# Kernel tuning notes

Hardware: AMD Instinct MI355X
Metric: run time of the kernel (lower is better)

## Reference

```python
import jax, jax.numpy as jnp
import numpy as np

B, E, H, T = 16384, 1024, 16, 256  # batch, embed_dim, num_heads, tabular_dim
HD = E // H  # head_dim


def _mha_seq1(q, kv, Wqkv, bqkv, Wo, bo):
    """nn.MultiheadAttention with query/key/value of seq_len 1 (batch_first).
    q, kv: [B, E]; Wqkv: [3E, E]; bqkv: [3E]; Wo: [E, E]; bo: [E]."""
    Wq, Wk, Wv = jnp.split(Wqkv, 3, axis=0)
    bq, bk, bv = jnp.split(bqkv, 3)
    qp = (q @ Wq.T + bq).reshape(-1, H, HD)   # [B, H, HD]
    kp = (kv @ Wk.T + bk).reshape(-1, H, HD)
    vp = (kv @ Wv.T + bv).reshape(-1, H, HD)
    scores = jnp.sum(qp * kp, axis=-1, keepdims=True) * (1.0 / HD ** 0.5)  # [B, H, 1]
    w = jax.nn.softmax(scores, axis=-1)       # softmax over 1 key -> all ones
    out = (w * vp).reshape(-1, E)             # [B, E]
    return out @ Wo.T + bo


def setup_inputs() -> dict:
    key = jax.random.key(0)
    ks = jax.random.split(key, 16)
    s_e = 1.0 / E ** 0.5
    s_t = 1.0 / T ** 0.5
    return {
        "text_features": jax.random.normal(ks[0], (B, E), jnp.float32),
        "ecg_features": jax.random.normal(ks[1], (B, E), jnp.float32),
        "tabular_features": jax.random.normal(ks[2], (B, T), jnp.float32),
        "Wc_text": jax.random.uniform(ks[3], (E, T), jnp.float32, -s_t, s_t),
        "bc_text": jax.random.uniform(ks[4], (E,), jnp.float32, -s_t, s_t),
        "Wc_ecg": jax.random.uniform(ks[5], (E, T), jnp.float32, -s_t, s_t),
        "bc_ecg": jax.random.uniform(ks[6], (E,), jnp.float32, -s_t, s_t),
        "Wqkv_a": jax.random.uniform(ks[7], (3 * E, E), jnp.float32, -s_e, s_e),
        "bqkv_a": jnp.zeros((3 * E,), jnp.float32),
        "Wo_a": jax.random.uniform(ks[8], (E, E), jnp.float32, -s_e, s_e),
        "bo_a": jnp.zeros((E,), jnp.float32),
        "Wqkv_b": jax.random.uniform(ks[9], (3 * E, E), jnp.float32, -s_e, s_e),
        "bqkv_b": jnp.zeros((3 * E,), jnp.float32),
        "Wo_b": jax.random.uniform(ks[10], (E, E), jnp.float32, -s_e, s_e),
        "bo_b": jnp.zeros((E,), jnp.float32),
    }


def reference(text_features, ecg_features, tabular_features,
              Wc_text, bc_text, Wc_ecg, bc_ecg,
              Wqkv_a, bqkv_a, Wo_a, bo_a,
              Wqkv_b, bqkv_b, Wo_b, bo_b):
    text_scale = jax.nn.sigmoid(tabular_features @ Wc_text.T + bc_text)
    ecg_scale = jax.nn.sigmoid(tabular_features @ Wc_ecg.T + bc_ecg)
    text_query = text_features * text_scale
    ecg_query = ecg_features * ecg_scale
    attn_a = _mha_seq1(text_query, ecg_features, Wqkv_a, bqkv_a, Wo_a, bo_a)
    attn_b = _mha_seq1(ecg_query, text_features, Wqkv_b, bqkv_b, Wo_b, bo_b)
    return jnp.concatenate([attn_a, attn_b], axis=-1)
```

## Files before the change

kernel.cpp:

```cpp
#include <hip/hip_runtime.h>
#include <hip/hip_bf16.h>
#include <stdint.h>

typedef __bf16 bf16_t;
typedef bf16_t bf16x8 __attribute__((ext_vector_type(8)));
typedef bf16_t bf16x4 __attribute__((ext_vector_type(4)));
typedef float  f32x4  __attribute__((ext_vector_type(4)));

#define E_DIM 1024
#define B_ROWS 16384

__device__ __forceinline__ void gload_lds16(const void* g, void* l) {
    __builtin_amdgcn_global_load_lds(
        (const __attribute__((address_space(1))) void*)g,
        (__attribute__((address_space(3))) void*)l,
        16, 0, 0);
}

__global__ __launch_bounds__(256) void cvt_w2_k(const float* __restrict__ Wo_a,
                                                const float* __restrict__ Wo_b,
                                                bf16_t* __restrict__ out) {
    const int n4 = (E_DIM * E_DIM) / 4;
    int i = blockIdx.x * blockDim.x + threadIdx.x;
    const float* src = (i < n4) ? Wo_a : Wo_b;
    int j = (i < n4) ? i : i - n4;
    f32x4 v = ((const f32x4*)src)[j];
    bf16x4 o;
    o[0] = (bf16_t)v[0]; o[1] = (bf16_t)v[1];
    o[2] = (bf16_t)v[2]; o[3] = (bf16_t)v[3];
    ((bf16x4*)out)[i] = o;
}

__global__ __launch_bounds__(256) void transpose_cvt2_k(const float* __restrict__ Wqkv_a,
                                                        const float* __restrict__ Wqkv_b,
                                                        bf16_t* __restrict__ out) {
    const size_t MAT = (size_t)E_DIM * E_DIM;
    int b = blockIdx.x;
    int ms = b >> 8;
    const float* in = (ms ? Wqkv_b : Wqkv_a) + 2 * MAT;
    bf16_t* o = out + (size_t)ms * MAT;
    int bb = b & 255;
    __shared__ float t[64][65];
    int bx = bb & 15;
    int by = bb >> 4;
    int j0 = by * 64, k0 = bx * 64;
    int tid = threadIdx.x;
#pragma unroll
    for (int p = 0; p < 4; ++p) {
        int u = tid + 256 * p;
        int r = u >> 4, c4 = u & 15;
        f32x4 v = *(const f32x4*)(in + (size_t)(j0 + r) * E_DIM + k0 + c4 * 4);
        t[r][c4 * 4 + 0] = v[0]; t[r][c4 * 4 + 1] = v[1];
        t[r][c4 * 4 + 2] = v[2]; t[r][c4 * 4 + 3] = v[3];
    }
    __syncthreads();
#pragma unroll
    for (int p = 0; p < 4; ++p) {
        int u = tid + 256 * p;
        int r = u >> 4, c4 = u & 15;
        bf16x4 ov;
        ov[0] = (bf16_t)t[c4 * 4 + 0][r];
        ov[1] = (bf16_t)t[c4 * 4 + 1][r];
        ov[2] = (bf16_t)t[c4 * 4 + 2][r];
        ov[3] = (bf16_t)t[c4 * 4 + 3][r];
        *(bf16x4*)(o + (size_t)(k0 + r) * E_DIM + j0 + c4 * 4) = ov;
    }
}

__global__ void fuse_bias2_k(const float* __restrict__ Wo_a, const float* __restrict__ bqkv_a,
                             const float* __restrict__ bo_a,
                             const float* __restrict__ Wo_b, const float* __restrict__ bqkv_b,
                             const float* __restrict__ bo_b, float* __restrict__ beff) {
    int idx = blockIdx.x;
    int sel = idx >> 10;
    int i = idx & 1023;
    const float* Wo = sel ? Wo_b : Wo_a;
    const float* bv = (sel ? bqkv_b : bqkv_a) + 2 * E_DIM;
    const float* bo = sel ? bo_b : bo_a;
    float s = 0.f;
    for (int j = threadIdx.x; j < E_DIM; j += 64)
        s += Wo[(size_t)i * E_DIM + j] * bv[j];
#pragma unroll
    for (int o = 32; o > 0; o >>= 1) s += __shfl_down(s, o);
    if (threadIdx.x == 0) beff[sel * E_DIM + i] = s + bo[i];
}

__global__ __launch_bounds__(256, 2) void fuse_gemm_k(const bf16_t* __restrict__ WoB,
                                                      const bf16_t* __restrict__ WvT,
                                                      bf16_t* __restrict__ Weff) {
    const size_t MAT = (size_t)E_DIM * E_DIM;
    int bid = blockIdx.x;
    int ms = bid >> 6;
    int t  = bid & 63;
    int mt = t >> 3, nt = t & 7;
    const bf16_t* A  = WoB + (size_t)ms * MAT;
    const bf16_t* Bm = WvT + (size_t)ms * MAT;
    bf16_t*       C  = Weff + (size_t)ms * MAT;
    int m0 = mt * 128, n0 = nt * 128;

    __shared__ __align__(16) bf16_t As[128][64];
    __shared__ __align__(16) bf16_t Bs[128][64];

    int tid = threadIdx.x;
    int lane = tid & 63;
    int wid = tid >> 6;
    int wrow = (wid >> 1) * 64;
    int wcol = (wid & 1) * 64;
    int cl = lane & 15;
    int rg = lane >> 4;

    f32x4 acc[4][4] = {};

    for (int kt = 0; kt < 16; ++kt) {
#pragma unroll
        for (int i = 0; i < 4; ++i) {
            int chunk = i * 256 + wid * 64 + lane;
            int row = chunk >> 3;
            int kk8 = (chunk & 7) * 8;
            char* la = (char*)(&As[0][0]) + (size_t)(i * 256 + wid * 64) * 16;
            char* lb = (char*)(&Bs[0][0]) + (size_t)(i * 256 + wid * 64) * 16;
            gload_lds16(A  + (size_t)(m0 + row) * E_DIM + kt * 64 + kk8, la);
            gload_lds16(Bm + (size_t)(n0 + row) * E_DIM + kt * 64 + kk8, lb);
        }
        __syncthreads();
#pragma unroll
        for (int ks = 0; ks < 2; ++ks) {
            int kk = ks * 32 + rg * 8;
            bf16x8 af[4], bq[4];
#pragma unroll
            for (int m = 0; m < 4; ++m) af[m] = *(const bf16x8*)(&As[wrow + m * 16 + cl][kk]);
#pragma unroll
            for (int n = 0; n < 4; ++n) bq[n] = *(const bf16x8*)(&Bs[wcol + n * 16 + cl][kk]);
#pragma unroll
            for (int m = 0; m < 4; ++m)
#pragma unroll
                for (int n = 0; n < 4; ++n)
                    acc[m][n] = __builtin_amdgcn_mfma_f32_16x16x32_bf16(af[m], bq[n], acc[m][n], 0, 0, 0);
        }
        __syncthreads();
    }

#pragma unroll
    for (int m = 0; m < 4; ++m) {
        int r = m0 + wrow + m * 16 + rg * 4;
#pragma unroll
        for (int n = 0; n < 4; ++n) {
            int c = n0 + wcol + n * 16 + cl;
#pragma unroll
            for (int j = 0; j < 4; ++j)
                C[(size_t)(r + j) * E_DIM + c] = (bf16_t)acc[m][n][j];
        }
    }
}

__global__ __launch_bounds__(256) void cvt_x2_k(const float* __restrict__ ecg,
                                                const float* __restrict__ text,
                                                bf16_t* __restrict__ out) {
    const int half = (B_ROWS * E_DIM) / 8;
    const int total = 2 * half;
    int stride = gridDim.x * blockDim.x;
    for (int i = blockIdx.x * blockDim.x + threadIdx.x; i < total; i += stride) {
        const float* src = (i < half) ? ecg : text;
        int j = (i < half) ? i : i - half;
        f32x4 lo = ((const f32x4*)src)[2 * j];
        f32x4 hi = ((const f32x4*)src)[2 * j + 1];
        bf16x8 v;
        v[0] = (bf16_t)lo[0]; v[1] = (bf16_t)lo[1]; v[2] = (bf16_t)lo[2]; v[3] = (bf16_t)lo[3];
        v[4] = (bf16_t)hi[0]; v[5] = (bf16_t)hi[1]; v[6] = (bf16_t)hi[2]; v[7] = (bf16_t)hi[3];
        ((bf16x8*)out)[i] = v;
    }
}

#define VMW(n) asm volatile("s_waitcnt vmcnt(" #n ")" ::: "memory")
#define BAR()  __builtin_amdgcn_s_barrier()

__global__ __launch_bounds__(512, 2) void main_gemm_256_k(const bf16_t* __restrict__ Xb,
                                                          const bf16_t* __restrict__ Weff,
                                                          const float* __restrict__ beff,
                                                          float* __restrict__ out) {
    const size_t MAT  = (size_t)E_DIM * E_DIM;
    const size_t XMAT = (size_t)B_ROWS * E_DIM;

    int bid = blockIdx.x;
    int wg = (bid & 7) * 64 + (bid >> 3);
    int nt = wg & 7;
    int mt = wg >> 3;
    int sel = nt >> 2;
    int n0 = (nt & 3) * 256;
    int m0 = mt * 256;

    const bf16_t* gA = Xb + (size_t)sel * XMAT + (size_t)m0 * E_DIM;
    const bf16_t* gB = Weff + (size_t)sel * MAT + (size_t)n0 * E_DIM;
    const float*  bb = beff + sel * E_DIM;

    __shared__ __align__(16) bf16_t sA[2][256 * 64];
    __shared__ __align__(16) bf16_t sB[2][256 * 64];

    int tid  = threadIdx.x;
    int lane = tid & 63;
    int wid  = tid >> 6;
    int wr = wid >> 2;
    int wc = wid & 3;
    int cl = lane & 15;
    int rg = lane >> 4;
    int wr16cl = wr * 16 + cl;
    int wc16cl = wc * 16 + cl;

    int c0 = tid, c1 = 512 + tid;
    int r0 = c0 >> 3, r1 = c1 >> 3;
    int go0 = r0 * E_DIM + (((c0 & 7) * 8) ^ ((r0 & 7) << 3));
    int go1 = r1 * E_DIM + (((c1 & 7) * 8) ^ ((r1 & 7) << 3));
    int ld0 = c0 * 8, ld1 = c1 * 8;

    int koff0 = (rg * 8) ^ ((cl & 7) << 3);
    int koff1 = (32 + rg * 8) ^ ((cl & 7) << 3);

    f32x4 acc[8][4] = {};
    bf16x8 af[4][2], bq[2][2];

#define STAGE_A(kt, h, prt) do { \
    gload_lds16(gA + (size_t)((h) * 128) * E_DIM + (kt) * 64 + go0, &sA[prt][(h) * 8192 + ld0]); \
    gload_lds16(gA + (size_t)((h) * 128) * E_DIM + (kt) * 64 + go1, &sA[prt][(h) * 8192 + ld1]); } while (0)
#define STAGE_B(kt, h, prt) do { \
    gload_lds16(gB + (size_t)((h) * 128) * E_DIM + (kt) * 64 + go0, &sB[prt][(h) * 8192 + ld0]); \
    gload_lds16(gB + (size_t)((h) * 128) * E_DIM + (kt) * 64 + go1, &sB[prt][(h) * 8192 + ld1]); } while (0)
#define RD_A(p, mh) do { _Pragma("unroll") for (int m = 0; m < 4; ++m) { \
    af[m][0] = *(const bf16x8*)(&sA[p][((mh) * 128 + m * 32 + wr16cl) * 64 + koff0]); \
    af[m][1] = *(const bf16x8*)(&sA[p][((mh) * 128 + m * 32 + wr16cl) * 64 + koff1]); } } while (0)
#define RD_B(p, nh) do { _Pragma("unroll") for (int n = 0; n < 2; ++n) { \
    bq[n][0] = *(const bf16x8*)(&sB[p][((nh) * 128 + n * 64 + wc16cl) * 64 + koff0]); \
    bq[n][1] = *(const bf16x8*)(&sB[p][((nh) * 128 + n * 64 + wc16cl) * 64 + koff1]); } } while (0)
#define MM(mh, nh) do { __builtin_amdgcn_s_setprio(1); \
    _Pragma("unroll") for (int m = 0; m < 4; ++m) _Pragma("unroll") for (int n = 0; n < 2; ++n) { \
        acc[(mh) * 4 + m][(nh) * 2 + n] = __builtin_amdgcn_mfma_f32_16x16x32_bf16(af[m][0], bq[n][0], acc[(mh) * 4 + m][(nh) * 2 + n], 0, 0, 0); \
        acc[(mh) * 4 + m][(nh) * 2 + n] = __builtin_amdgcn_mfma_f32_16x16x32_bf16(af[m][1], bq[n][1], acc[(mh) * 4 + m][(nh) * 2 + n], 0, 0, 0); } \
    __builtin_amdgcn_s_setprio(0); } while (0)

    STAGE_A(0, 0, 0); STAGE_B(0, 0, 0); STAGE_B(0, 1, 0); STAGE_A(0, 1, 0);
    VMW(4);
    BAR();

#pragma unroll
    for (int t = 0; t < 16; ++t) {
        const int p = t & 1, pn = p ^ 1;
        RD_A(p, 0); RD_B(p, 0);
        if (t < 15) { STAGE_A(t + 1, 0, pn); VMW(4); } else { VMW(2); }
        BAR();
        MM(0, 0);
        BAR();
        RD_B(p, 1);
        if (t < 15) { STAGE_B(t + 1, 0, pn); VMW(4); } else { VMW(0); }
        BAR();
        MM(0, 1);
        BAR();
        RD_A(p, 1);
        if (t < 15) STAGE_B(t + 1, 1, pn);
        BAR();
        MM(1, 1);
        BAR();
        RD_B(p, 0);
        if (t < 15) { STAGE_A(t + 1, 1, pn); VMW(4); }
        BAR();
        MM(1, 0);
        BAR();
    }

#pragma unroll
    for (int mi = 0; mi < 8; ++mi) {
        int r = m0 + mi * 32 + wr * 16 + rg * 4;
#pragma unroll
        for (int n = 0; n < 4; ++n) {
            int ch = n0 + n * 64 + wc16cl;
            float bias = bb[ch];
            size_t gc = (size_t)sel * E_DIM + ch;
#pragma unroll
            for (int j = 0; j < 4; ++j)
                out[(size_t)(r + j) * (2 * E_DIM) + gc] = acc[mi][n][j] + bias;
        }
    }
#undef STAGE_A
#undef STAGE_B
#undef RD_A
#undef RD_B
#undef MM
}

extern "C" void kernel_launch(void* const* d_in, const int* in_sizes, int n_in,
                              void* d_out, int out_size, void* d_ws, size_t ws_size,
                              hipStream_t stream) {
    const float* text   = (const float*)d_in[0];
    const float* ecg    = (const float*)d_in[1];
    const float* Wqkv_a = (const float*)d_in[7];
    const float* bqkv_a = (const float*)d_in[8];
    const float* Wo_a   = (const float*)d_in[9];
    const float* bo_a   = (const float*)d_in[10];
    const float* Wqkv_b = (const float*)d_in[11];
    const float* bqkv_b = (const float*)d_in[12];
    const float* Wo_b   = (const float*)d_in[13];
    const float* bo_b   = (const float*)d_in[14];

    const size_t MAT  = (size_t)E_DIM * E_DIM;
    const size_t XMAT = (size_t)B_ROWS * E_DIM;
    bf16_t* WoB  = (bf16_t*)d_ws;
    bf16_t* WvT  = WoB + 2 * MAT;
    bf16_t* Weff = WvT + 2 * MAT;
    float*  beff = (float*)(Weff + 2 * MAT);
    bf16_t* Xb   = (bf16_t*)(beff + 2 * E_DIM);

    cvt_x2_k<<<4096, 256, 0, stream>>>(ecg, text, Xb);
    cvt_w2_k<<<2048, 256, 0, stream>>>(Wo_a, Wo_b, WoB);
    transpose_cvt2_k<<<512, 256, 0, stream>>>(Wqkv_a, Wqkv_b, WvT);
    fuse_gemm_k<<<128, 256, 0, stream>>>(WoB, WvT, Weff);
    fuse_bias2_k<<<2048, 64, 0, stream>>>(Wo_a, bqkv_a, bo_a, Wo_b, bqkv_b, bo_b, beff);
    main_gemm_256_k<<<512, 512, 0, stream>>>(Xb, Weff, beff, (float*)d_out);
}
```

Baseline: 158.5 us.

## Fuse activation bf16 conversion into main GEMM and merge weight-prep kernels

The main GEMM now loads fp32 text/ecg rows straight into registers two k-tiles ahead, converts them to bf16 and writes them into swizzled LDS. This removes the separate activation-conversion kernel and its bf16 round-trip through global memory. The three small weight-prep kernels (Wo convert, Wv transpose, bias fold) are merged into one launch to cut launch overhead. In exchange, A traffic into the GEMM doubles in bytes, register pressure rises from the prefetch buffers, and the pipeline schedule is reworked.

```diff
diff --git a/kernel.cpp b/kernel.cpp
--- a/kernel.cpp
+++ b/kernel.cpp
@@ -17,72 +17,74 @@
         16, 0, 0);
 }
 
-__global__ __launch_bounds__(256) void cvt_w2_k(const float* __restrict__ Wo_a,
-                                                const float* __restrict__ Wo_b,
-                                                bf16_t* __restrict__ out) {
-    const int n4 = (E_DIM * E_DIM) / 4;
-    int i = blockIdx.x * blockDim.x + threadIdx.x;
-    const float* src = (i < n4) ? Wo_a : Wo_b;
-    int j = (i < n4) ? i : i - n4;
-    f32x4 v = ((const f32x4*)src)[j];
-    bf16x4 o;
-    o[0] = (bf16_t)v[0]; o[1] = (bf16_t)v[1];
-    o[2] = (bf16_t)v[2]; o[3] = (bf16_t)v[3];
-    ((bf16x4*)out)[i] = o;
-}
-
-__global__ __launch_bounds__(256) void transpose_cvt2_k(const float* __restrict__ Wqkv_a,
-                                                        const float* __restrict__ Wqkv_b,
-                                                        bf16_t* __restrict__ out) {
+__global__ __launch_bounds__(256) void prep_misc_k(const float* __restrict__ Wqkv_a,
+                                                   const float* __restrict__ bqkv_a,
+                                                   const float* __restrict__ Wo_a,
+                                                   const float* __restrict__ bo_a,
+                                                   const float* __restrict__ Wqkv_b,
+                                                   const float* __restrict__ bqkv_b,
+                                                   const float* __restrict__ Wo_b,
+                                                   const float* __restrict__ bo_b,
+                                                   bf16_t* __restrict__ WoB,
+                                                   bf16_t* __restrict__ WvT,
+                                                   float* __restrict__ beff) {
     const size_t MAT = (size_t)E_DIM * E_DIM;
+    __shared__ float t[64][65];
     int b = blockIdx.x;
-    int ms = b >> 8;
-    const float* in = (ms ? Wqkv_b : Wqkv_a) + 2 * MAT;
-    bf16_t* o = out + (size_t)ms * MAT;
-    int bb = b & 255;
-    __shared__ float t[64][65];
-    int bx = bb & 15;
-    int by = bb >> 4;
-    int j0 = by * 64, k0 = bx * 64;
     int tid = threadIdx.x;
-#pragma unroll
-    for (int p = 0; p < 4; ++p) {
-        int u = tid + 256 * p;
-        int r = u >> 4, c4 = u & 15;
-        f32x4 v = *(const f32x4*)(in + (size_t)(j0 + r) * E_DIM + k0 + c4 * 4);
-        t[r][c4 * 4 + 0] = v[0]; t[r][c4 * 4 + 1] = v[1];
-        t[r][c4 * 4 + 2] = v[2]; t[r][c4 * 4 + 3] = v[3];
-    }
-    __syncthreads();
-#pragma unroll
-    for (int p = 0; p < 4; ++p) {
-        int u = tid + 256 * p;
-        int r = u >> 4, c4 = u & 15;
-        bf16x4 ov;
-        ov[0] = (bf16_t)t[c4 * 4 + 0][r];
-        ov[1] = (bf16_t)t[c4 * 4 + 1][r];
-        ov[2] = (bf16_t)t[c4 * 4 + 2][r];
-        ov[3] = (bf16_t)t[c4 * 4 + 3][r];
-        *(bf16x4*)(o + (size_t)(k0 + r) * E_DIM + j0 + c4 * 4) = ov;
-    }
-}
-
-__global__ void fuse_bias2_k(const float* __restrict__ Wo_a, const float* __restrict__ bqkv_a,
-                             const float* __restrict__ bo_a,
-                             const float* __restrict__ Wo_b, const float* __restrict__ bqkv_b,
-                             const float* __restrict__ bo_b, float* __restrict__ beff) {
-    int idx = blockIdx.x;
-    int sel = idx >> 10;
-    int i = idx & 1023;
-    const float* Wo = sel ? Wo_b : Wo_a;
-    const float* bv = (sel ? bqkv_b : bqkv_a) + 2 * E_DIM;
-    const float* bo = sel ? bo_b : bo_a;
-    float s = 0.f;
-    for (int j = threadIdx.x; j < E_DIM; j += 64)
-        s += Wo[(size_t)i * E_DIM + j] * bv[j];
-#pragma unroll
-    for (int o = 32; o > 0; o >>= 1) s += __shfl_down(s, o);
-    if (threadIdx.x == 0) beff[sel * E_DIM + i] = s + bo[i];
+    if (b < 2048) {
+        const int n4 = (int)(MAT / 4);
+        int i = b * 256 + tid;
+        const float* src = (i < n4) ? Wo_a : Wo_b;
+        int j = (i < n4) ? i : i - n4;
+        f32x4 v = ((const f32x4*)src)[j];
+        bf16x4 o;
+        o[0] = (bf16_t)v[0]; o[1] = (bf16_t)v[1];
+        o[2] = (bf16_t)v[2]; o[3] = (bf16_t)v[3];
+        ((bf16x4*)WoB)[i] = o;
+    } else if (b < 2560) {
+        int x = b - 2048;
+        int ms = x >> 8;
+        const float* in = (ms ? Wqkv_b : Wqkv_a) + 2 * MAT;
+        bf16_t* o = WvT + (size_t)ms * MAT;
+        int bb = x & 255;
+        int bx = bb & 15, by = bb >> 4;
+        int j0 = by * 64, k0 = bx * 64;
+#pragma unroll
+        for (int p = 0; p < 4; ++p) {
+            int u = tid + 256 * p;
+            int r = u >> 4, c4 = u & 15;
+            f32x4 v = *(const f32x4*)(in + (size_t)(j0 + r) * E_DIM + k0 + c4 * 4);
+            t[r][c4 * 4 + 0] = v[0]; t[r][c4 * 4 + 1] = v[1];
+            t[r][c4 * 4 + 2] = v[2]; t[r][c4 * 4 + 3] = v[3];
+        }
+        __syncthreads();
+#pragma unroll
+        for (int p = 0; p < 4; ++p) {
+            int u = tid + 256 * p;
+            int r = u >> 4, c4 = u & 15;
+            bf16x4 ov;
+            ov[0] = (bf16_t)t[c4 * 4 + 0][r];
+            ov[1] = (bf16_t)t[c4 * 4 + 1][r];
+            ov[2] = (bf16_t)t[c4 * 4 + 2][r];
+            ov[3] = (bf16_t)t[c4 * 4 + 3][r];
+            *(bf16x4*)(o + (size_t)(k0 + r) * E_DIM + j0 + c4 * 4) = ov;
+        }
+    } else {
+        int idx = (b - 2560) * 4 + (tid >> 6);
+        int lane = tid & 63;
+        int sel = idx >> 10;
+        int i = idx & 1023;
+        const float* Wo = sel ? Wo_b : Wo_a;
+        const float* bv = (sel ? bqkv_b : bqkv_a) + 2 * E_DIM;
+        const float* bo = sel ? bo_b : bo_a;
+        float s = 0.f;
+        for (int j = lane; j < E_DIM; j += 64)
+            s += Wo[(size_t)i * E_DIM + j] * bv[j];
+#pragma unroll
+        for (int o = 32; o > 0; o >>= 1) s += __shfl_down(s, o);
+        if (lane == 0) beff[sel * E_DIM + i] = s + bo[i];
+    }
 }
 
 __global__ __launch_bounds__(256, 2) void fuse_gemm_k(const bf16_t* __restrict__ WoB,
@@ -153,33 +155,16 @@
     }
 }
 
-__global__ __launch_bounds__(256) void cvt_x2_k(const float* __restrict__ ecg,
-                                                const float* __restrict__ text,
-                                                bf16_t* __restrict__ out) {
-    const int half = (B_ROWS * E_DIM) / 8;
-    const int total = 2 * half;
-    int stride = gridDim.x * blockDim.x;
-    for (int i = blockIdx.x * blockDim.x + threadIdx.x; i < total; i += stride) {
-        const float* src = (i < half) ? ecg : text;
-        int j = (i < half) ? i : i - half;
-        f32x4 lo = ((const f32x4*)src)[2 * j];
-        f32x4 hi = ((const f32x4*)src)[2 * j + 1];
-        bf16x8 v;
-        v[0] = (bf16_t)lo[0]; v[1] = (bf16_t)lo[1]; v[2] = (bf16_t)lo[2]; v[3] = (bf16_t)lo[3];
-        v[4] = (bf16_t)hi[0]; v[5] = (bf16_t)hi[1]; v[6] = (bf16_t)hi[2]; v[7] = (bf16_t)hi[3];
-        ((bf16x8*)out)[i] = v;
-    }
-}
-
-#define VMW(n) asm volatile("s_waitcnt vmcnt(" #n ")" ::: "memory")
-#define BAR()  __builtin_amdgcn_s_barrier()
-
-__global__ __launch_bounds__(512, 2) void main_gemm_256_k(const bf16_t* __restrict__ Xb,
+#define VMW(n)  asm volatile("s_waitcnt vmcnt(" #n ")" ::: "memory")
+#define LGKM0() asm volatile("s_waitcnt lgkmcnt(0)" ::: "memory")
+#define BAR()   __builtin_amdgcn_s_barrier()
+
+__global__ __launch_bounds__(512, 2) void main_gemm_f32_k(const float* __restrict__ text,
+                                                          const float* __restrict__ ecg,
                                                           const bf16_t* __restrict__ Weff,
                                                           const float* __restrict__ beff,
                                                           float* __restrict__ out) {
-    const size_t MAT  = (size_t)E_DIM * E_DIM;
-    const size_t XMAT = (size_t)B_ROWS * E_DIM;
+    const size_t MAT = (size_t)E_DIM * E_DIM;
 
     int bid = blockIdx.x;
     int wg = (bid & 7) * 64 + (bid >> 3);
@@ -189,7 +174,7 @@
     int n0 = (nt & 3) * 256;
     int m0 = mt * 256;
 
-    const bf16_t* gA = Xb + (size_t)sel * XMAT + (size_t)m0 * E_DIM;
+    const float*  gA = (sel ? text : ecg) + (size_t)m0 * E_DIM;
     const bf16_t* gB = Weff + (size_t)sel * MAT + (size_t)n0 * E_DIM;
     const float*  bb = beff + sel * E_DIM;
 
@@ -208,61 +193,73 @@
 
     int c0 = tid, c1 = 512 + tid;
     int r0 = c0 >> 3, r1 = c1 >> 3;
-    int go0 = r0 * E_DIM + (((c0 & 7) * 8) ^ ((r0 & 7) << 3));
-    int go1 = r1 * E_DIM + (((c1 & 7) * 8) ^ ((r1 & 7) << 3));
+    int sc0 = ((c0 & 7) * 8) ^ ((r0 & 7) << 3);
+    int go0 = r0 * E_DIM + sc0;
+    int go1 = r1 * E_DIM + sc0;
     int ld0 = c0 * 8, ld1 = c1 * 8;
 
     int koff0 = (rg * 8) ^ ((cl & 7) << 3);
     int koff1 = (32 + rg * 8) ^ ((cl & 7) << 3);
 
     f32x4 acc[8][4] = {};
-    bf16x8 af[4][2], bq[2][2];
-
-#define STAGE_A(kt, h, prt) do { \
-    gload_lds16(gA + (size_t)((h) * 128) * E_DIM + (kt) * 64 + go0, &sA[prt][(h) * 8192 + ld0]); \
-    gload_lds16(gA + (size_t)((h) * 128) * E_DIM + (kt) * 64 + go1, &sA[prt][(h) * 8192 + ld1]); } while (0)
+    bf16x8 af[4][2], bqs[2][2], bq[2][2];
+    f32x4 pa[2][4];
+
 #define STAGE_B(kt, h, prt) do { \
     gload_lds16(gB + (size_t)((h) * 128) * E_DIM + (kt) * 64 + go0, &sB[prt][(h) * 8192 + ld0]); \
     gload_lds16(gB + (size_t)((h) * 128) * E_DIM + (kt) * 64 + go1, &sB[prt][(h) * 8192 + ld1]); } while (0)
+#define LOAD_A(kt, h) do { \
+    const float* _p0 = gA + (size_t)((h) * 128 + r0) * E_DIM + (kt) * 64 + sc0; \
+    const float* _p1 = gA + (size_t)((h) * 128 + 64 + r0) * E_DIM + (kt) * 64 + sc0; \
+    pa[h][0] = *(const f32x4*)_p0; pa[h][1] = *(const f32x4*)(_p0 + 4); \
+    pa[h][2] = *(const f32x4*)_p1; pa[h][3] = *(const f32x4*)(_p1 + 4); } while (0)
+#define CVT_A(h, prt) do { \
+    bf16x8 _v0, _v1; \
+    _v0[0] = (bf16_t)pa[h][0][0]; _v0[1] = (bf16_t)pa[h][0][1]; \
+    _v0[2] = (bf16_t)pa[h][0][2]; _v0[3] = (bf16_t)pa[h][0][3]; \
+    _v0[4] = (bf16_t)pa[h][1][0]; _v0[5] = (bf16_t)pa[h][1][1]; \
+    _v0[6] = (bf16_t)pa[h][1][2]; _v0[7] = (bf16_t)pa[h][1][3]; \
+    _v1[0] = (bf16_t)pa[h][2][0]; _v1[1] = (bf16_t)pa[h][2][1]; \
+    _v1[2] = (bf16_t)pa[h][2][2]; _v1[3] = (bf16_t)pa[h][2][3]; \
+    _v1[4] = (bf16_t)pa[h][3][0]; _v1[5] = (bf16_t)pa[h][3][1]; \
+    _v1[6] = (bf16_t)pa[h][3][2]; _v1[7] = (bf16_t)pa[h][3][3]; \
+    *(bf16x8*)(&sA[prt][(h) * 8192 + ld0]) = _v0; \
+    *(bf16x8*)(&sA[prt][(h) * 8192 + ld1]) = _v1; } while (0)
 #define RD_A(p, mh) do { _Pragma("unroll") for (int m = 0; m < 4; ++m) { \
     af[m][0] = *(const bf16x8*)(&sA[p][((mh) * 128 + m * 32 + wr16cl) * 64 + koff0]); \
     af[m][1] = *(const bf16x8*)(&sA[p][((mh) * 128 + m * 32 + wr16cl) * 64 + koff1]); } } while (0)
-#define RD_B(p, nh) do { _Pragma("unroll") for (int n = 0; n < 2; ++n) { \
-    bq[n][0] = *(const bf16x8*)(&sB[p][((nh) * 128 + n * 64 + wc16cl) * 64 + koff0]); \
-    bq[n][1] = *(const bf16x8*)(&sB[p][((nh) * 128 + n * 64 + wc16cl) * 64 + koff1]); } } while (0)
-#define MM(mh, nh) do { __builtin_amdgcn_s_setprio(1); \
+#define RD_B(p, nh, DST) do { _Pragma("unroll") for (int n = 0; n < 2; ++n) { \
+    DST[n][0] = *(const bf16x8*)(&sB[p][((nh) * 128 + n * 64 + wc16cl) * 64 + koff0]); \
+    DST[n][1] = *(const bf16x8*)(&sB[p][((nh) * 128 + n * 64 + wc16cl) * 64 + koff1]); } } while (0)
+#define MM(mh, nh, BQ) do { __builtin_amdgcn_s_setprio(1); \
     _Pragma("unroll") for (int m = 0; m < 4; ++m) _Pragma("unroll") for (int n = 0; n < 2; ++n) { \
-        acc[(mh) * 4 + m][(nh) * 2 + n] = __builtin_amdgcn_mfma_f32_16x16x32_bf16(af[m][0], bq[n][0], acc[(mh) * 4 + m][(nh) * 2 + n], 0, 0, 0); \
-        acc[(mh) * 4 + m][(nh) * 2 + n] = __builtin_amdgcn_mfma_f32_16x16x32_bf16(af[m][1], bq[n][1], acc[(mh) * 4 + m][(nh) * 2 + n], 0, 0, 0); } \
+        acc[(mh) * 4 + m][(nh) * 2 + n] = __builtin_amdgcn_mfma_f32_16x16x32_bf16(af[m][0], BQ[n][0], acc[(mh) * 4 + m][(nh) * 2 + n], 0, 0, 0); \
+        acc[(mh) * 4 + m][(nh) * 2 + n] = __builtin_amdgcn_mfma_f32_16x16x32_bf16(af[m][1], BQ[n][1], acc[(mh) * 4 + m][(nh) * 2 + n], 0, 0, 0); } \
     __builtin_amdgcn_s_setprio(0); } while (0)
 
-    STAGE_A(0, 0, 0); STAGE_B(0, 0, 0); STAGE_B(0, 1, 0); STAGE_A(0, 1, 0);
-    VMW(4);
+    LOAD_A(0, 0); LOAD_A(0, 1);
+    STAGE_B(0, 0, 0); STAGE_B(0, 1, 0);
+    CVT_A(0, 0); CVT_A(1, 0);
+    LOAD_A(1, 0); LOAD_A(1, 1);
+    VMW(8);
+    LGKM0();
     BAR();
 
 #pragma unroll
     for (int t = 0; t < 16; ++t) {
         const int p = t & 1, pn = p ^ 1;
-        RD_A(p, 0); RD_B(p, 0);
-        if (t < 15) { STAGE_A(t + 1, 0, pn); VMW(4); } else { VMW(2); }
-        BAR();
-        MM(0, 0);
-        BAR();
-        RD_B(p, 1);
-        if (t < 15) { STAGE_B(t + 1, 0, pn); VMW(4); } else { VMW(0); }
-        BAR();
-        MM(0, 1);
-        BAR();
+        RD_A(p, 0); RD_B(p, 0, bqs);
+        BAR(); MM(0, 0, bqs); BAR();
+        RD_B(p, 1, bq);
+        if (t < 15) { STAGE_B(t + 1, 0, pn); CVT_A(0, pn); }
+        BAR(); MM(0, 1, bq); BAR();
         RD_A(p, 1);
-        if (t < 15) STAGE_B(t + 1, 1, pn);
-        BAR();
-        MM(1, 1);
-        BAR();
-        RD_B(p, 0);
-        if (t < 15) { STAGE_A(t + 1, 1, pn); VMW(4); }
-        BAR();
-        MM(1, 0);
-        BAR();
+        if (t < 15) { STAGE_B(t + 1, 1, pn); CVT_A(1, pn); }
+        BAR(); MM(1, 1, bq); BAR();
+        if (t < 14) { LOAD_A(t + 2, 0); LOAD_A(t + 2, 1); VMW(8); }
+        else if (t == 14) { VMW(0); }
+        LGKM0();
+        BAR(); MM(1, 0, bqs); BAR();
     }
 
 #pragma unroll
@@ -278,8 +275,9 @@
                 out[(size_t)(r + j) * (2 * E_DIM) + gc] = acc[mi][n][j] + bias;
         }
     }
-#undef STAGE_A
 #undef STAGE_B
+#undef LOAD_A
+#undef CVT_A
 #undef RD_A
 #undef RD_B
 #undef MM
@@ -299,18 +297,15 @@
     const float* Wo_b   = (const float*)d_in[13];
     const float* bo_b   = (const float*)d_in[14];
 
-    const size_t MAT  = (size_t)E_DIM * E_DIM;
-    const size_t XMAT = (size_t)B_ROWS * E_DIM;
+    const size_t MAT = (size_t)E_DIM * E_DIM;
     bf16_t* WoB  = (bf16_t*)d_ws;
     bf16_t* WvT  = WoB + 2 * MAT;
     bf16_t* Weff = WvT + 2 * MAT;
     float*  beff = (float*)(Weff + 2 * MAT);
-    bf16_t* Xb   = (bf16_t*)(beff + 2 * E_DIM);
-
-    cvt_x2_k<<<4096, 256, 0, stream>>>(ecg, text, Xb);
-    cvt_w2_k<<<2048, 256, 0, stream>>>(Wo_a, Wo_b, WoB);
-    transpose_cvt2_k<<<512, 256, 0, stream>>>(Wqkv_a, Wqkv_b, WvT);
+
+    prep_misc_k<<<3072, 256, 0, stream>>>(Wqkv_a, bqkv_a, Wo_a, bo_a,
+                                          Wqkv_b, bqkv_b, Wo_b, bo_b,
+                                          WoB, WvT, beff);
     fuse_gemm_k<<<128, 256, 0, stream>>>(WoB, WvT, Weff);
-    fuse_bias2_k<<<2048, 64, 0, stream>>>(Wo_a, bqkv_a, bo_a, Wo_b, bqkv_b, bo_b, beff);
-    main_gemm_256_k<<<512, 512, 0, stream>>>(Xb, Weff, beff, (float*)d_out);
-}
+    main_gemm_f32_k<<<512, 512, 0, stream>>>(text, ecg, Weff, beff, (float*)d_out);
+}
```

Result: no change. 160.3 us (+1.1%).

## Merge weight-prep and activation-convert kernels into fewer launches

Applied to the files above, without the earlier changes.

Merges the Wo conversion, Wv transpose-convert and fused-bias kernels into one block-range-dispatched prep kernel. It also runs the activation bf16 conversion in the same launch as the Weff fusion GEMM, so the small 128-block GEMM overlaps the bandwidth-bound conversion. This cuts launches from six to three and removes serial gaps. The cost is that the conversion blocks now carry the GEMM's LDS allocation and launch bounds, which can lower their occupancy.

```diff
diff --git a/kernel.cpp b/kernel.cpp
--- a/kernel.cpp
+++ b/kernel.cpp
@@ -17,79 +17,107 @@
         16, 0, 0);
 }
 
-__global__ __launch_bounds__(256) void cvt_w2_k(const float* __restrict__ Wo_a,
+__global__ __launch_bounds__(256) void prep_w_k(const float* __restrict__ Wqkv_a,
+                                                const float* __restrict__ bqkv_a,
+                                                const float* __restrict__ Wo_a,
+                                                const float* __restrict__ bo_a,
+                                                const float* __restrict__ Wqkv_b,
+                                                const float* __restrict__ bqkv_b,
                                                 const float* __restrict__ Wo_b,
-                                                bf16_t* __restrict__ out) {
-    const int n4 = (E_DIM * E_DIM) / 4;
-    int i = blockIdx.x * blockDim.x + threadIdx.x;
-    const float* src = (i < n4) ? Wo_a : Wo_b;
-    int j = (i < n4) ? i : i - n4;
-    f32x4 v = ((const f32x4*)src)[j];
-    bf16x4 o;
-    o[0] = (bf16_t)v[0]; o[1] = (bf16_t)v[1];
-    o[2] = (bf16_t)v[2]; o[3] = (bf16_t)v[3];
-    ((bf16x4*)out)[i] = o;
-}
-
-__global__ __launch_bounds__(256) void transpose_cvt2_k(const float* __restrict__ Wqkv_a,
-                                                        const float* __restrict__ Wqkv_b,
-                                                        bf16_t* __restrict__ out) {
+                                                const float* __restrict__ bo_b,
+                                                bf16_t* __restrict__ WoB,
+                                                bf16_t* __restrict__ WvT,
+                                                float* __restrict__ beff) {
     const size_t MAT = (size_t)E_DIM * E_DIM;
+    __shared__ float t[64][65];
     int b = blockIdx.x;
-    int ms = b >> 8;
-    const float* in = (ms ? Wqkv_b : Wqkv_a) + 2 * MAT;
-    bf16_t* o = out + (size_t)ms * MAT;
-    int bb = b & 255;
-    __shared__ float t[64][65];
-    int bx = bb & 15;
-    int by = bb >> 4;
-    int j0 = by * 64, k0 = bx * 64;
     int tid = threadIdx.x;
-#pragma unroll
-    for (int p = 0; p < 4; ++p) {
-        int u = tid + 256 * p;
-        int r = u >> 4, c4 = u & 15;
-        f32x4 v = *(const f32x4*)(in + (size_t)(j0 + r) * E_DIM + k0 + c4 * 4);
-        t[r][c4 * 4 + 0] = v[0]; t[r][c4 * 4 + 1] = v[1];
-        t[r][c4 * 4 + 2] = v[2]; t[r][c4 * 4 + 3] = v[3];
-    }
-    __syncthreads();
-#pragma unroll
-    for (int p = 0; p < 4; ++p) {
-        int u = tid + 256 * p;
-        int r = u >> 4, c4 = u & 15;
-        bf16x4 ov;
-        ov[0] = (bf16_t)t[c4 * 4 + 0][r];
-        ov[1] = (bf16_t)t[c4 * 4 + 1][r];
-        ov[2] = (bf16_t)t[c4 * 4 + 2][r];
-        ov[3] = (bf16_t)t[c4 * 4 + 3][r];
-        *(bf16x4*)(o + (size_t)(k0 + r) * E_DIM + j0 + c4 * 4) = ov;
-    }
-}
-
-__global__ void fuse_bias2_k(const float* __restrict__ Wo_a, const float* __restrict__ bqkv_a,
-                             const float* __restrict__ bo_a,
-                             const float* __restrict__ Wo_b, const float* __restrict__ bqkv_b,
-                             const float* __restrict__ bo_b, float* __restrict__ beff) {
-    int idx = blockIdx.x;
-    int sel = idx >> 10;
-    int i = idx & 1023;
-    const float* Wo = sel ? Wo_b : Wo_a;
-    const float* bv = (sel ? bqkv_b : bqkv_a) + 2 * E_DIM;
-    const float* bo = sel ? bo_b : bo_a;
-    float s = 0.f;
-    for (int j = threadIdx.x; j < E_DIM; j += 64)
-        s += Wo[(size_t)i * E_DIM + j] * bv[j];
-#pragma unroll
-    for (int o = 32; o > 0; o >>= 1) s += __shfl_down(s, o);
-    if (threadIdx.x == 0) beff[sel * E_DIM + i] = s + bo[i];
-}
-
-__global__ __launch_bounds__(256, 2) void fuse_gemm_k(const bf16_t* __restrict__ WoB,
-                                                      const bf16_t* __restrict__ WvT,
-                                                      bf16_t* __restrict__ Weff) {
+    if (b < 2048) {
+        const int n4 = (int)(MAT / 4);
+        int i = b * 256 + tid;
+        const float* src = (i < n4) ? Wo_a : Wo_b;
+        int j = (i < n4) ? i : i - n4;
+        f32x4 v = ((const f32x4*)src)[j];
+        bf16x4 o;
+        o[0] = (bf16_t)v[0]; o[1] = (bf16_t)v[1];
+        o[2] = (bf16_t)v[2]; o[3] = (bf16_t)v[3];
+        ((bf16x4*)WoB)[i] = o;
+    } else if (b < 2560) {
+        int x = b - 2048;
+        int ms = x >> 8;
+        const float* in = (ms ? Wqkv_b : Wqkv_a) + 2 * MAT;
+        bf16_t* o = WvT + (size_t)ms * MAT;
+        int bb = x & 255;
+        int bx = bb & 15, by = bb >> 4;
+        int j0 = by * 64, k0 = bx * 64;
+#pragma unroll
+        for (int p = 0; p < 4; ++p) {
+            int u = tid + 256 * p;
+            int r = u >> 4, c4 = u & 15;
+            f32x4 v = *(const f32x4*)(in + (size_t)(j0 + r) * E_DIM + k0 + c4 * 4);
+            t[r][c4 * 4 + 0] = v[0]; t[r][c4 * 4 + 1] = v[1];
+            t[r][c4 * 4 + 2] = v[2]; t[r][c4 * 4 + 3] = v[3];
+        }
+        __syncthreads();
+#pragma unroll
+        for (int p = 0; p < 4; ++p) {
+            int u = tid + 256 * p;
+            int r = u >> 4, c4 = u & 15;
+            bf16x4 ov;
+            ov[0] = (bf16_t)t[c4 * 4 + 0][r];
+            ov[1] = (bf16_t)t[c4 * 4 + 1][r];
+            ov[2] = (bf16_t)t[c4 * 4 + 2][r];
+            ov[3] = (bf16_t)t[c4 * 4 + 3][r];
+            *(bf16x4*)(o + (size_t)(k0 + r) * E_DIM + j0 + c4 * 4) = ov;
+        }
+    } else {
+        int idx = (b - 2560) * 4 + (tid >> 6);
+        int lane = tid & 63;
+        int sel = idx >> 10;
+        int i = idx & 1023;
+        const float* Wo = sel ? Wo_b : Wo_a;
+        const float* bv = (sel ? bqkv_b : bqkv_a) + 2 * E_DIM;
+        const float* bo = sel ? bo_b : bo_a;
+        float s = 0.f;
+        for (int j = lane; j < E_DIM; j += 64)
+            s += Wo[(size_t)i * E_DIM + j] * bv[j];
+#pragma unroll
+        for (int o = 32; o > 0; o >>= 1) s += __shfl_down(s, o);
+        if (lane == 0) beff[sel * E_DIM + i] = s + bo[i];
+    }
+}
+
+__global__ __launch_bounds__(256, 2) void combo_k(const float* __restrict__ ecg,
+                                                  const float* __restrict__ text,
+                                                  bf16_t* __restrict__ Xb,
+                                                  const bf16_t* __restrict__ WoB,
+                                                  const bf16_t* __restrict__ WvT,
+                                                  bf16_t* __restrict__ Weff) {
     const size_t MAT = (size_t)E_DIM * E_DIM;
-    int bid = blockIdx.x;
+    __shared__ __align__(16) bf16_t As[128][64];
+    __shared__ __align__(16) bf16_t Bs[128][64];
+
+    int b = blockIdx.x;
+    int tid = threadIdx.x;
+
+    if (b < 2048) {
+        const int half = (B_ROWS * E_DIM) / 8;
+        const int total = 2 * half;
+        const int stride = 2048 * 256;
+        for (int i = b * 256 + tid; i < total; i += stride) {
+            const float* src = (i < half) ? ecg : text;
+            int j = (i < half) ? i : i - half;
+            f32x4 lo = ((const f32x4*)src)[2 * j];
+            f32x4 hi = ((const f32x4*)src)[2 * j + 1];
+            bf16x8 v;
+            v[0] = (bf16_t)lo[0]; v[1] = (bf16_t)lo[1]; v[2] = (bf16_t)lo[2]; v[3] = (bf16_t)lo[3];
+            v[4] = (bf16_t)hi[0]; v[5] = (bf16_t)hi[1]; v[6] = (bf16_t)hi[2]; v[7] = (bf16_t)hi[3];
+            ((bf16x8*)Xb)[i] = v;
+        }
+        return;
+    }
+
+    int bid = b - 2048;
     int ms = bid >> 6;
     int t  = bid & 63;
     int mt = t >> 3, nt = t & 7;
@@ -98,10 +126,6 @@
     bf16_t*       C  = Weff + (size_t)ms * MAT;
     int m0 = mt * 128, n0 = nt * 128;
 
-    __shared__ __align__(16) bf16_t As[128][64];
-    __shared__ __align__(16) bf16_t Bs[128][64];
-
-    int tid = threadIdx.x;
     int lane = tid & 63;
     int wid = tid >> 6;
     int wrow = (wid >> 1) * 64;
@@ -150,24 +174,6 @@
             for (int j = 0; j < 4; ++j)
                 C[(size_t)(r + j) * E_DIM + c] = (bf16_t)acc[m][n][j];
         }
-    }
-}
-
-__global__ __launch_bounds__(256) void cvt_x2_k(const float* __restrict__ ecg,
-                                                const float* __restrict__ text,
-                                                bf16_t* __restrict__ out) {
-    const int half = (B_ROWS * E_DIM) / 8;
-    const int total = 2 * half;
-    int stride = gridDim.x * blockDim.x;
-    for (int i = blockIdx.x * blockDim.x + threadIdx.x; i < total; i += stride) {
-        const float* src = (i < half) ? ecg : text;
-        int j = (i < half) ? i : i - half;
-        f32x4 lo = ((const f32x4*)src)[2 * j];
-        f32x4 hi = ((const f32x4*)src)[2 * j + 1];
-        bf16x8 v;
-        v[0] = (bf16_t)lo[0]; v[1] = (bf16_t)lo[1]; v[2] = (bf16_t)lo[2]; v[3] = (bf16_t)lo[3];
-        v[4] = (bf16_t)hi[0]; v[5] = (bf16_t)hi[1]; v[6] = (bf16_t)hi[2]; v[7] = (bf16_t)hi[3];
-        ((bf16x8*)out)[i] = v;
     }
 }
 
@@ -307,10 +313,9 @@
     float*  beff = (float*)(Weff + 2 * MAT);
     bf16_t* Xb   = (bf16_t*)(beff + 2 * E_DIM);
 
-    cvt_x2_k<<<4096, 256, 0, stream>>>(ecg, text, Xb);
-    cvt_w2_k<<<2048, 256, 0, stream>>>(Wo_a, Wo_b, WoB);
-    transpose_cvt2_k<<<512, 256, 0, stream>>>(Wqkv_a, Wqkv_b, WvT);
-    fuse_gemm_k<<<128, 256, 0, stream>>>(WoB, WvT, Weff);
-    fuse_bias2_k<<<2048, 64, 0, stream>>>(Wo_a, bqkv_a, bo_a, Wo_b, bqkv_b, bo_b, beff);
+    prep_w_k<<<3072, 256, 0, stream>>>(Wqkv_a, bqkv_a, Wo_a, bo_a,
+                                       Wqkv_b, bqkv_b, Wo_b, bo_b,
+                                       WoB, WvT, beff);
+    combo_k<<<2176, 256, 0, stream>>>(ecg, text, Xb, WoB, WvT, Weff);
     main_gemm_256_k<<<512, 512, 0, stream>>>(Xb, Weff, beff, (float*)d_out);
 }
```

Result: faster. 148.8 us (-6.1%).
